# Optimization experiments

Hardware: AMD Instinct MI355X
Metric: run time of the kernel (lower is better)

Reference implementation:

```python
import jax, jax.numpy as jnp
import numpy as np

_EPS = 1e-12  # torch F.normalize eps


def _normalize(x):
    # x: [B, N, 3]; matches torch.nn.functional.normalize(x, dim=2)
    norm = jnp.linalg.norm(x, axis=2, keepdims=True)
    return x / jnp.maximum(norm, _EPS)


def setup_inputs() -> dict:
    key = jax.random.key(0)
    k1, k2 = jax.random.split(key)
    xyz1 = jax.random.normal(k1, (8, 4096, 6), dtype=jnp.float32)
    xyz2 = jax.random.normal(k2, (8, 4096, 6), dtype=jnp.float32)
    return {"xyz1": xyz1, "xyz2": xyz2}


def reference(xyz1, xyz2):
    p1 = xyz1[:, :, :3]  # [B, N, 3]
    p2 = xyz2[:, :, :3]  # [B, M, 3]
    n1 = xyz1[:, :, 3:]  # [B, N, 3]
    n2 = xyz2[:, :, 3:]  # [B, M, 3]

    # Pairwise squared L2: |a|^2 + |b|^2 - 2 a.b  -> [B, N, M]
    sq1 = jnp.sum(p1 * p1, axis=2)  # [B, N]
    sq2 = jnp.sum(p2 * p2, axis=2)  # [B, M]
    cross = jnp.einsum('bnd,bmd->bnm', p1, p2)
    d = sq1[:, :, None] + sq2[:, None, :] - 2.0 * cross  # [B, N, M]

    dist1 = jnp.min(d, axis=2)      # [B, N] NN of each p1 in p2
    idx1 = jnp.argmin(d, axis=2)    # [B, N]
    dist2 = jnp.min(d, axis=1)      # [B, M] NN of each p2 in p1
    idx2 = jnp.argmin(d, axis=1)    # [B, M]

    # Gather matched normals
    t1 = jnp.take_along_axis(n2, idx1[:, :, None], axis=1)  # [B, N, 3]
    t2 = jnp.take_along_axis(n1, idx2[:, :, None], axis=1)  # [B, M, 3]

    nd1 = jnp.sum((_normalize(n1) - _normalize(t1)) ** 2, axis=2)  # [B, N]
    nd2 = jnp.sum((_normalize(n2) - _normalize(t2)) ** 2, axis=2)  # [B, M]

    return jnp.mean(dist1) + jnp.mean(dist2) + jnp.mean(nd1) + jnp.mean(nd2)
```

## Files before the change

kernel.cpp:

```cpp
#include <hip/hip_runtime.h>
#include <cstdint>

#define NB 8
#define NP 4096
#define THREADS 256
#define Q 8
#define CHUNK (THREADS * Q)
#define NCHUNK (NP / CHUNK)
#define G 4


template <int SEGV>
__global__ __launch_bounds__(THREADS) void chamfer_argmin(
    const float* __restrict__ xyz1, const float* __restrict__ xyz2,
    unsigned int* __restrict__ part, float* __restrict__ out)
{
    const int TSEG = NP / SEGV;
    __shared__ float4 tgt[NP / 16];

    unsigned int x = blockIdx.x;
    if (x == 0 && threadIdx.x == 0) out[0] = 0.0f;
    int seg   = x & (SEGV - 1);
    int chunk = (x / SEGV) & (NCHUNK - 1);
    int b     = (x / (SEGV * NCHUNK)) & 7;
    int dir   = x / (SEGV * NCHUNK * 8);

    const float* qset = dir ? xyz2 : xyz1;
    const float* tset = dir ? xyz1 : xyz2;

    int tbase = seg * TSEG;
    for (int t0 = threadIdx.x; t0 < TSEG; t0 += THREADS) {
        const float* src = tset + ((size_t)b * NP + tbase + t0) * 6;
        float tx = src[0], ty = src[1], tz = src[2];
        tgt[t0] = make_float4(tx, ty, tz, -0.5f * (tx * tx + ty * ty + tz * tz));
    }
    __syncthreads();

    float qx[Q], qy[Q], qz[Q], qq[Q], bs[Q];
    unsigned int bi[Q];
    int qbase = chunk * CHUNK + threadIdx.x;
    #pragma unroll
    for (int i = 0; i < Q; ++i) {
        const float* src = qset + ((size_t)b * NP + qbase + i * THREADS) * 6;
        qx[i] = src[0]; qy[i] = src[1]; qz[i] = src[2];
        qq[i] = qx[i] * qx[i] + qy[i] * qy[i] + qz[i] * qz[i];
        bs[i] = -3.4e38f;
        bi[i] = 0u;
    }

    #pragma unroll 2
    for (int k = 0; k < TSEG; k += G) {
        float4 t0 = tgt[k + 0];
        float4 t1 = tgt[k + 1];
        float4 t2 = tgt[k + 2];
        float4 t3 = tgt[k + 3];
        #pragma unroll
        for (int i = 0; i < Q; ++i) {
            float s0 = fmaf(t0.x, qx[i], fmaf(t0.y, qy[i], fmaf(t0.z, qz[i], t0.w)));
            float s1 = fmaf(t1.x, qx[i], fmaf(t1.y, qy[i], fmaf(t1.z, qz[i], t1.w)));
            float s2 = fmaf(t2.x, qx[i], fmaf(t2.y, qy[i], fmaf(t2.z, qz[i], t2.w)));
            float s3 = fmaf(t3.x, qx[i], fmaf(t3.y, qy[i], fmaf(t3.z, qz[i], t3.w)));
            float m  = fmaxf(fmaxf(s0, s1), fmaxf(s2, s3));
            if (m > bs[i]) { bs[i] = m; bi[i] = (unsigned int)k; }
        }
    }

    unsigned int* slot =
        part + (((size_t)(dir * NB + b) * SEGV + seg) * NP) + qbase;
    #pragma unroll
    for (int i = 0; i < Q; ++i) {
        int k = (int)bi[i];
        float4 t0 = tgt[k + 0];
        float4 t1 = tgt[k + 1];
        float4 t2 = tgt[k + 2];
        float4 t3 = tgt[k + 3];
        float s0 = fmaf(t0.x, qx[i], fmaf(t0.y, qy[i], fmaf(t0.z, qz[i], t0.w)));
        float s1 = fmaf(t1.x, qx[i], fmaf(t1.y, qy[i], fmaf(t1.z, qz[i], t1.w)));
        float s2 = fmaf(t2.x, qx[i], fmaf(t2.y, qy[i], fmaf(t2.z, qz[i], t2.w)));
        unsigned int j  = (unsigned int)(tbase + k);
        unsigned int jj = j + 3;
        jj = (s2 == bs[i]) ? j + 2 : jj;
        jj = (s1 == bs[i]) ? j + 1 : jj;
        jj = (s0 == bs[i]) ? j     : jj;
        float d = fmaxf(fmaf(-2.0f, bs[i], qq[i]), 0.0f);
        slot[i * THREADS] = (__float_as_uint(d) & 0xFFFFF000u) | jj;
    }
}

template <int SEGV>
__global__ __launch_bounds__(256) void chamfer_finish(
    const float* __restrict__ xyz1, const float* __restrict__ xyz2,
    const unsigned int* __restrict__ part, float* __restrict__ out)
{
    int gid = blockIdx.x * 256 + threadIdx.x;
    int q   = gid & (NP - 1);
    int db  = gid >> 12;
    int b   = db & 7;
    int dir = db >> 3;

    const unsigned int* base = part + ((size_t)db * SEGV) * NP + q;
    unsigned int p = 0xFFFFFFFFu;
    #pragma unroll
    for (int s = 0; s < SEGV; ++s) p = min(p, base[(size_t)s * NP]);

    const float* qset = dir ? xyz2 : xyz1;
    const float* tset = dir ? xyz1 : xyz2;

    float dist = __uint_as_float(p & 0xFFFFF000u);
    int j = (int)(p & 0xFFFu);

    const float* nq = qset + ((size_t)b * NP + q) * 6 + 3;
    const float* nt = tset + ((size_t)b * NP + j) * 6 + 3;
    float ax = nq[0], ay = nq[1], az = nq[2];
    float bx = nt[0], by = nt[1], bz = nt[2];

    float na = fmaxf(sqrtf(ax * ax + ay * ay + az * az), 1e-12f);
    float nb = fmaxf(sqrtf(bx * bx + by * by + bz * bz), 1e-12f);
    float ra = 1.0f / na, rb = 1.0f / nb;
    float dx = ax * ra - bx * rb;
    float dy = ay * ra - by * rb;
    float dz = az * ra - bz * rb;
    float nd = dx * dx + dy * dy + dz * dz;

    float contrib = (dist + nd) * (1.0f / 32768.0f);

    for (int off = 32; off > 0; off >>= 1)
        contrib += __shfl_down(contrib, off, 64);
    __shared__ float wsum[4];
    if ((threadIdx.x & 63) == 0) wsum[threadIdx.x >> 6] = contrib;
    __syncthreads();
    if (threadIdx.x == 0)
        atomicAdd(out, wsum[0] + wsum[1] + wsum[2] + wsum[3]);
}

extern "C" void kernel_launch(void* const* d_in, const int* in_sizes, int n_in,
                              void* d_out, int out_size, void* d_ws, size_t ws_size,
                              hipStream_t stream) {
    const float* xyz1 = (const float*)d_in[0];
    const float* xyz2 = (const float*)d_in[1];
    float* out = (float*)d_out;
    unsigned int* part = (unsigned int*)d_ws;

    size_t need32 = (size_t)2 * NB * 32 * NP * sizeof(unsigned int);
    if (ws_size >= need32) {
        chamfer_argmin<32><<<2 * NB * NCHUNK * 32, THREADS, 0, stream>>>(xyz1, xyz2, part, out);
        chamfer_finish<32><<<(2 * NB * NP) / 256, 256, 0, stream>>>(xyz1, xyz2, part, out);
    } else {
        chamfer_argmin<16><<<2 * NB * NCHUNK * 16, THREADS, 0, stream>>>(xyz1, xyz2, part, out);
        chamfer_finish<16><<<(2 * NB * NP) / 256, 256, 0, stream>>>(xyz1, xyz2, part, out);
    }
}
```

Before: 87.47 us.

## Widen argmin target group to 8 and split finish reduction across waves

The argmin inner loop now evaluates 8 targets per group and folds the running best into a single max tree, updating the index only when the best changes. This cuts compare and branch overhead per target. The finish kernel now gives each query 4 waves, each reducing a quarter of the segment partials, then merges them through shared memory, which spreads the partial loads over more threads. It uses 4x as many blocks, only one wave per block does the normal math, and atomics are issued per wave instead of per block.

```diff
diff --git a/kernel.cpp b/kernel.cpp
--- a/kernel.cpp
+++ b/kernel.cpp
@@ -7,7 +7,7 @@
 #define Q 8
 #define CHUNK (THREADS * Q)
 #define NCHUNK (NP / CHUNK)
-#define G 4
+#define G 8
 
 
 template <int SEGV>
@@ -54,14 +54,27 @@
         float4 t1 = tgt[k + 1];
         float4 t2 = tgt[k + 2];
         float4 t3 = tgt[k + 3];
+        float4 t4 = tgt[k + 4];
+        float4 t5 = tgt[k + 5];
+        float4 t6 = tgt[k + 6];
+        float4 t7 = tgt[k + 7];
         #pragma unroll
         for (int i = 0; i < Q; ++i) {
             float s0 = fmaf(t0.x, qx[i], fmaf(t0.y, qy[i], fmaf(t0.z, qz[i], t0.w)));
             float s1 = fmaf(t1.x, qx[i], fmaf(t1.y, qy[i], fmaf(t1.z, qz[i], t1.w)));
             float s2 = fmaf(t2.x, qx[i], fmaf(t2.y, qy[i], fmaf(t2.z, qz[i], t2.w)));
             float s3 = fmaf(t3.x, qx[i], fmaf(t3.y, qy[i], fmaf(t3.z, qz[i], t3.w)));
-            float m  = fmaxf(fmaxf(s0, s1), fmaxf(s2, s3));
-            if (m > bs[i]) { bs[i] = m; bi[i] = (unsigned int)k; }
+            float s4 = fmaf(t4.x, qx[i], fmaf(t4.y, qy[i], fmaf(t4.z, qz[i], t4.w)));
+            float s5 = fmaf(t5.x, qx[i], fmaf(t5.y, qy[i], fmaf(t5.z, qz[i], t5.w)));
+            float s6 = fmaf(t6.x, qx[i], fmaf(t6.y, qy[i], fmaf(t6.z, qz[i], t6.w)));
+            float s7 = fmaf(t7.x, qx[i], fmaf(t7.y, qy[i], fmaf(t7.z, qz[i], t7.w)));
+            float old = bs[i];
+            float m1 = fmaxf(fmaxf(s0, s1), s2);
+            float m2 = fmaxf(fmaxf(s3, s4), s5);
+            float m3 = fmaxf(fmaxf(s6, s7), old);
+            float bn = fmaxf(fmaxf(m1, m2), m3);
+            bs[i] = bn;
+            if (bn != old) bi[i] = (unsigned int)k;
         }
     }
 
@@ -70,18 +83,14 @@
     #pragma unroll
     for (int i = 0; i < Q; ++i) {
         int k = (int)bi[i];
-        float4 t0 = tgt[k + 0];
-        float4 t1 = tgt[k + 1];
-        float4 t2 = tgt[k + 2];
-        float4 t3 = tgt[k + 3];
-        float s0 = fmaf(t0.x, qx[i], fmaf(t0.y, qy[i], fmaf(t0.z, qz[i], t0.w)));
-        float s1 = fmaf(t1.x, qx[i], fmaf(t1.y, qy[i], fmaf(t1.z, qz[i], t1.w)));
-        float s2 = fmaf(t2.x, qx[i], fmaf(t2.y, qy[i], fmaf(t2.z, qz[i], t2.w)));
         unsigned int j  = (unsigned int)(tbase + k);
-        unsigned int jj = j + 3;
-        jj = (s2 == bs[i]) ? j + 2 : jj;
-        jj = (s1 == bs[i]) ? j + 1 : jj;
-        jj = (s0 == bs[i]) ? j     : jj;
+        unsigned int jj = j + 7;
+        #pragma unroll
+        for (int t = 6; t >= 0; --t) {
+            float4 tv = tgt[k + t];
+            float s = fmaf(tv.x, qx[i], fmaf(tv.y, qy[i], fmaf(tv.z, qz[i], tv.w)));
+            jj = (s == bs[i]) ? j + (unsigned int)t : jj;
+        }
         float d = fmaxf(fmaf(-2.0f, bs[i], qq[i]), 0.0f);
         slot[i * THREADS] = (__float_as_uint(d) & 0xFFFFF000u) | jj;
     }
@@ -92,16 +101,24 @@
     const float* __restrict__ xyz1, const float* __restrict__ xyz2,
     const unsigned int* __restrict__ part, float* __restrict__ out)
 {
-    int gid = blockIdx.x * 256 + threadIdx.x;
-    int q   = gid & (NP - 1);
-    int db  = gid >> 12;
+    constexpr int SPS = SEGV / 4;
+    int ql  = threadIdx.x & 63;
+    int sub = threadIdx.x >> 6;
+    int db  = blockIdx.x >> 6;
+    int q   = ((blockIdx.x & 63) << 6) + ql;
     int b   = db & 7;
     int dir = db >> 3;
 
-    const unsigned int* base = part + ((size_t)db * SEGV) * NP + q;
+    const unsigned int* base = part + ((size_t)db * SEGV + sub * SPS) * NP + q;
     unsigned int p = 0xFFFFFFFFu;
     #pragma unroll
-    for (int s = 0; s < SEGV; ++s) p = min(p, base[(size_t)s * NP]);
+    for (int s = 0; s < SPS; ++s) p = min(p, base[(size_t)s * NP]);
+
+    __shared__ unsigned int red[3][64];
+    if (sub) { red[sub - 1][ql] = p; }
+    __syncthreads();
+    if (sub) return;
+    p = min(min(p, red[0][ql]), min(red[1][ql], red[2][ql]));
 
     const float* qset = dir ? xyz2 : xyz1;
     const float* tset = dir ? xyz1 : xyz2;
@@ -126,11 +143,7 @@
 
     for (int off = 32; off > 0; off >>= 1)
         contrib += __shfl_down(contrib, off, 64);
-    __shared__ float wsum[4];
-    if ((threadIdx.x & 63) == 0) wsum[threadIdx.x >> 6] = contrib;
-    __syncthreads();
-    if (threadIdx.x == 0)
-        atomicAdd(out, wsum[0] + wsum[1] + wsum[2] + wsum[3]);
+    if (ql == 0) atomicAdd(out, contrib);
 }
 
 extern "C" void kernel_launch(void* const* d_in, const int* in_sizes, int n_in,
@@ -144,9 +157,9 @@
     size_t need32 = (size_t)2 * NB * 32 * NP * sizeof(unsigned int);
     if (ws_size >= need32) {
         chamfer_argmin<32><<<2 * NB * NCHUNK * 32, THREADS, 0, stream>>>(xyz1, xyz2, part, out);
-        chamfer_finish<32><<<(2 * NB * NP) / 256, 256, 0, stream>>>(xyz1, xyz2, part, out);
+        chamfer_finish<32><<<16 * 64, 256, 0, stream>>>(xyz1, xyz2, part, out);
     } else {
         chamfer_argmin<16><<<2 * NB * NCHUNK * 16, THREADS, 0, stream>>>(xyz1, xyz2, part, out);
-        chamfer_finish<16><<<(2 * NB * NP) / 256, 256, 0, stream>>>(xyz1, xyz2, part, out);
+        chamfer_finish<16><<<16 * 64, 256, 0, stream>>>(xyz1, xyz2, part, out);
     }
 }
```

Result: slower. 98.06 us (+12.1%).
